# Optimization experiments

Measured on AMD Instinct MI355X. Metric: run time of the kernel, lower is better.

The kernel has to match this reference:

```python
import jax, jax.numpy as jnp
import numpy as np
from jax import lax

B_, CIN, COUT, H, W = 8, 64, 64, 64, 64
DIN, DSTATE, K, DTRANK = 128, 16, 4, 4  # d_inner=2*C, d_state=16, 4 scan dirs, dt_rank=ceil(64/16)


def setup_inputs():
    key = jax.random.key(0)
    ks = jax.random.split(key, 10)
    f = lambda k, s, sc=0.02: jax.random.normal(k, s, jnp.float32) * sc
    return {
        "x": jax.random.normal(ks[0], (B_, CIN, H, W), jnp.float32),
        "conv_w": f(ks[1], (COUT, CIN, 3, 3)),
        "conv_b": jnp.zeros((COUT,), jnp.float32),
        "gn_g": jnp.ones((COUT,), jnp.float32),
        "gn_b": jnp.zeros((COUT,), jnp.float32),
        "ln1_g": jnp.ones((COUT,), jnp.float32),
        "ln1_b": jnp.zeros((COUT,), jnp.float32),
        "in_proj_w": f(ks[2], (COUT, 2 * DIN)),
        "dw_w": f(ks[3], (DIN, 1, 3, 3)),
        "dw_b": jnp.zeros((DIN,), jnp.float32),
        "x_proj_w": f(ks[4], (K, DTRANK + 2 * DSTATE, DIN)),
        "dt_w": f(ks[5], (K, DIN, DTRANK)),
        "dt_b": f(ks[6], (K, DIN), 0.01),
        "A_logs": jnp.tile(jnp.log(jnp.arange(1, DSTATE + 1, dtype=jnp.float32)), (K, DIN, 1)),
        "Ds": jnp.ones((K, DIN), jnp.float32),
        "out_norm_g": jnp.ones((DIN,), jnp.float32),
        "out_norm_b": jnp.zeros((DIN,), jnp.float32),
        "out_proj_w": f(ks[7], (DIN, COUT)),
    }


def _ln(x, g, b, eps=1e-5):
    m = x.mean(-1, keepdims=True)
    v = ((x - m) ** 2).mean(-1, keepdims=True)
    return (x - m) * lax.rsqrt(v + eps) * g + b


def reference(x, conv_w, conv_b, gn_g, gn_b, ln1_g, ln1_b, in_proj_w, dw_w, dw_b,
              x_proj_w, dt_w, dt_b, A_logs, Ds, out_norm_g, out_norm_b, out_proj_w):
    # BasicConv2d: conv3x3 (stride 1, pad 1) + GroupNorm(2) + SiLU
    y = lax.conv_general_dilated(x, conv_w, (1, 1), [(1, 1), (1, 1)],
                                 dimension_numbers=("NCHW", "OIHW", "NCHW"))
    y = y + conv_b[None, :, None, None]
    Bb, C, Hh, Ww = y.shape
    yg = y.reshape(Bb, 2, C // 2, Hh, Ww)
    m = yg.mean((2, 3, 4), keepdims=True)
    v = ((yg - m) ** 2).mean((2, 3, 4), keepdims=True)
    y = ((yg - m) * lax.rsqrt(v + 1e-5)).reshape(Bb, C, Hh, Ww)
    y = y * gn_g[None, :, None, None] + gn_b[None, :, None, None]
    y = jax.nn.silu(y)
    # VSSBlock on NHWC: LN -> SS2D -> residual
    xb = y.transpose(0, 2, 3, 1)                       # (B,H,W,C)
    h = _ln(xb, ln1_g, ln1_b)
    xz = h @ in_proj_w                                 # (B,H,W,2*DIN)
    xm, z = jnp.split(xz, 2, axis=-1)
    xm = xm.transpose(0, 3, 1, 2)                      # (B,DIN,H,W)
    xm = lax.conv_general_dilated(xm, dw_w, (1, 1), [(1, 1), (1, 1)],
                                  dimension_numbers=("NCHW", "OIHW", "NCHW"),
                                  feature_group_count=DIN)
    xm = jax.nn.silu(xm + dw_b[None, :, None, None])
    L = Hh * Ww
    x1 = xm.reshape(Bb, DIN, L)                        # HW order
    x2 = xm.transpose(0, 1, 3, 2).reshape(Bb, DIN, L)  # WH order
    xs = jnp.stack([x1, x2], 1)
    xs = jnp.concatenate([xs, jnp.flip(xs, -1)], 1)    # (B,4,DIN,L)
    xdbl = jnp.einsum("bkdl,kcd->bkcl", xs, x_proj_w)
    dts, Bs, Cs = jnp.split(xdbl, [DTRANK, DTRANK + DSTATE], axis=2)
    dts = jnp.einsum("bkrl,kdr->bkdl", dts, dt_w)
    dt = jax.nn.softplus(dts + dt_b[None, :, :, None])  # (B,4,DIN,L)
    A = -jnp.exp(A_logs)                                # (K,DIN,DSTATE)
    # selective scan over L (time-major)
    u_t = xs.transpose(3, 0, 1, 2)
    dt_t = dt.transpose(3, 0, 1, 2)
    B_t = Bs.transpose(3, 0, 1, 2)
    C_t = Cs.transpose(3, 0, 1, 2)

    def step(hst, inp):
        u, d, Bc, Cc = inp
        hst = hst * jnp.exp(d[..., None] * A) + (d * u)[..., None] * Bc[:, :, None, :]
        return hst, jnp.einsum("bkdn,bkn->bkd", hst, Cc)

    h0 = jnp.zeros((Bb, K, DIN, DSTATE), xs.dtype)
    _, ys = lax.scan(step, h0, (u_t, dt_t, B_t, C_t))  # ys: (L,B,4,DIN)
    out_y = ys.transpose(1, 2, 3, 0) + Ds[None, :, :, None] * xs
    inv_y = jnp.flip(out_y[:, 2:4], -1)
    wh_y = out_y[:, 1].reshape(Bb, DIN, Ww, Hh).transpose(0, 1, 3, 2).reshape(Bb, DIN, L)
    invwh_y = inv_y[:, 1].reshape(Bb, DIN, Ww, Hh).transpose(0, 1, 3, 2).reshape(Bb, DIN, L)
    yv = out_y[:, 0] + inv_y[:, 0] + wh_y + invwh_y    # (B,DIN,L)
    yv = yv.transpose(0, 2, 1).reshape(Bb, Hh, Ww, DIN)
    yv = _ln(yv, out_norm_g, out_norm_b)
    yv = yv * jax.nn.silu(z)
    vss = xb + yv @ out_proj_w                          # VSSBlock residual
    return vss.transpose(0, 3, 1, 2) + y                # MambaDU residual
```

## Files before the change

### kernel.cpp

```cpp
#include <hip/hip_runtime.h>
#include <hip/hip_bf16.h>

#define BD   8
#define CD   64
#define HD   64
#define WD   64
#define LD   4096
#define DINN 128
#define KDIR 4
#define NST  16
#define L2E  1.442695040888963f

typedef const float* fp;

__device__ __forceinline__ float sigm(float x) { return 1.f / (1.f + __expf(-x)); }
__device__ __forceinline__ float softplusf(float x) {
    float e = __expf(-fabsf(x));
    return fmaxf(x, 0.f) + __logf(1.f + e);
}
__device__ __forceinline__ int pmap(int k, int l) {
    int m = (k & 2) ? (LD - 1 - l) : l;
    return (k & 1) ? (((m & 63) << 6) | (m >> 6)) : m;
}

__global__ __launch_bounds__(256) void k_conv(fp x, fp cw, fp cb, float* conv_out, float* gstats) {
    __shared__ float xt[64][3][68];
    __shared__ float red[4][4];
    int bx = blockIdx.x; int b = bx >> 6; int h = bx & 63;
    int t = threadIdx.x;
    for (int idx = t; idx < 64 * 3 * 64; idx += 256) {
        int ci = idx / 192, rem = idx % 192, r = rem >> 6, w = rem & 63;
        int hs = h + r - 1;
        float v = 0.f;
        if (hs >= 0 && hs < 64) v = x[((b * 64 + ci) * 64 + hs) * 64 + w];
        xt[ci][r][w + 1] = v;
    }
    for (int idx = t; idx < 64 * 3; idx += 256) {
        int ci = idx / 3, r = idx % 3;
        xt[ci][r][0] = 0.f; xt[ci][r][65] = 0.f; xt[ci][r][66] = 0.f; xt[ci][r][67] = 0.f;
    }
    __syncthreads();
    int co = t & 63, wq = t >> 6;
    float acc[16];
#pragma unroll
    for (int j = 0; j < 16; j++) acc[j] = 0.f;
    for (int ci = 0; ci < 64; ci++) {
        float wv[9];
        fp wp = cw + (co * 64 + ci) * 9;
#pragma unroll
        for (int q = 0; q < 9; q++) wv[q] = wp[q];
#pragma unroll
        for (int r = 0; r < 3; r++) {
            const float* row = &xt[ci][r][wq * 16];
            float xw[20];
#pragma unroll
            for (int q = 0; q < 5; q++) {
                float4 f = ((const float4*)row)[q];
                xw[4 * q] = f.x; xw[4 * q + 1] = f.y; xw[4 * q + 2] = f.z; xw[4 * q + 3] = f.w;
            }
#pragma unroll
            for (int j = 0; j < 16; j++)
                acc[j] += wv[r * 3 + 0] * xw[j] + wv[r * 3 + 1] * xw[j + 1] + wv[r * 3 + 2] * xw[j + 2];
        }
    }
    float bias = cb[co];
    __syncthreads();
    float* ot = &xt[0][0][0];
#pragma unroll
    for (int j = 0; j < 16; j++) ot[co * 64 + wq * 16 + j] = acc[j] + bias;
    __syncthreads();
    float ps0 = 0.f, pq0 = 0.f, ps1 = 0.f, pq1 = 0.f;
    for (int idx = t; idx < 4096; idx += 256) {
        int c2 = idx >> 6, w2 = idx & 63;
        float v = ot[idx];
        conv_out[((b * 64 + c2) * 64 + h) * 64 + w2] = v;
        bool g0 = c2 < 32;
        float v2 = v * v;
        ps0 += g0 ? v : 0.f; pq0 += g0 ? v2 : 0.f;
        ps1 += g0 ? 0.f : v; pq1 += g0 ? 0.f : v2;
    }
#pragma unroll
    for (int off = 32; off; off >>= 1) {
        ps0 += __shfl_xor(ps0, off); pq0 += __shfl_xor(pq0, off);
        ps1 += __shfl_xor(ps1, off); pq1 += __shfl_xor(pq1, off);
    }
    int wid = t >> 6;
    if ((t & 63) == 0) { red[wid][0] = ps0; red[wid][1] = pq0; red[wid][2] = ps1; red[wid][3] = pq1; }
    __syncthreads();
    if (t < 4) {
        float v = red[0][t] + red[1][t] + red[2][t] + red[3][t];
        atomicAdd(&gstats[b * 4 + t], v);
    }
}

__global__ __launch_bounds__(256) void k_gnapply(const float* conv_out, const float* gstats,
                                                 fp gng, fp gnb, float* y_nhwc) {
    __shared__ float tile[64][65];
    int bx = blockIdx.x; int b = bx >> 6; int p0 = (bx & 63) * 64;
    int t = threadIdx.x;
    const float invN = 1.f / (32.f * 4096.f);
    float s0 = gstats[b * 4 + 0], q0 = gstats[b * 4 + 1];
    float s1 = gstats[b * 4 + 2], q1 = gstats[b * 4 + 3];
    float m0 = s0 * invN, r0 = rsqrtf(q0 * invN - m0 * m0 + 1e-5f);
    float m1 = s1 * invN, r1 = rsqrtf(q1 * invN - m1 * m1 + 1e-5f);
    for (int idx = t; idx < 4096; idx += 256) {
        int c = idx >> 6, pi = idx & 63;
        float v = conv_out[(b * 64 + c) * LD + p0 + pi];
        float mean = (c < 32) ? m0 : m1, rstd = (c < 32) ? r0 : r1;
        v = (v - mean) * rstd * gng[c] + gnb[c];
        v = v * sigm(v);
        tile[c][pi] = v;
    }
    __syncthreads();
    for (int idx = t; idx < 4096; idx += 256) {
        int pi = idx >> 6, c = idx & 63;
        y_nhwc[(b * LD + p0 + pi) * 64 + c] = tile[c][pi];
    }
}

__global__ __launch_bounds__(256) void k_lninproj(const float* y_nhwc, fp lng, fp lnb, fp ipw,
                                                  float* xmc, float* zsil) {
    __shared__ float hn[4][64];
    int bp0 = blockIdx.x * 4;
    int t = threadIdx.x;
    int pix = t >> 6, lane = t & 63;
    {
        float v = y_nhwc[(bp0 + pix) * 64 + lane];
        float s = v, s2 = v * v;
#pragma unroll
        for (int off = 32; off; off >>= 1) { s += __shfl_xor(s, off); s2 += __shfl_xor(s2, off); }
        float mean = s * (1.f / 64.f);
        float rstd = rsqrtf(s2 * (1.f / 64.f) - mean * mean + 1e-5f);
        hn[pix][lane] = (v - mean) * rstd * lng[lane] + lnb[lane];
    }
    __syncthreads();
    float a0 = 0.f, a1 = 0.f, a2 = 0.f, a3 = 0.f;
    for (int c = 0; c < 64; c++) {
        float w = ipw[c * 256 + t];
        a0 += hn[0][c] * w; a1 += hn[1][c] * w; a2 += hn[2][c] * w; a3 += hn[3][c] * w;
    }
    float accv[4] = {a0, a1, a2, a3};
#pragma unroll
    for (int p = 0; p < 4; p++) {
        int bp = bp0 + p;
        float v = accv[p];
        if (t < 128) xmc[bp * 128 + t] = v;
        else         zsil[bp * 128 + (t - 128)] = v * sigm(v);
    }
}

__global__ __launch_bounds__(256) void k_dwconv(const float* xmc, fp dww, fp dwb, float* xm_dw) {
    int id = blockIdx.x * 256 + threadIdx.x;
    int d = id & 127, p = (id >> 7) & (LD - 1), b = id >> 19;
    int h = p >> 6, w = p & 63;
    float wv[9];
#pragma unroll
    for (int q = 0; q < 9; q++) wv[q] = dww[d * 9 + q];
    float acc = dwb[d];
#pragma unroll
    for (int i = 0; i < 3; i++) {
        int hs = h + i - 1; if (hs < 0 || hs > 63) continue;
#pragma unroll
        for (int j = 0; j < 3; j++) {
            int ws = w + j - 1; if (ws < 0 || ws > 63) continue;
            acc += xmc[((b << 12) + (hs << 6) + ws) * 128 + d] * wv[i * 3 + j];
        }
    }
    acc = acc * sigm(acc);
    xm_dw[id] = acc;
}

__global__ __launch_bounds__(192) void k_proj(const float* xm_dw, fp xpw, float* dts4, float* xBC) {
    __shared__ float u_lds[64 * 130];
    __shared__ float w_lds[128 * 40];
    int bx = blockIdx.x;
    int lt = bx & 63; int bk = bx >> 6; int k = bk & 3; int b = bk >> 2;
    int l0 = lt * 64;
    int t = threadIdx.x;
    for (int idx = t; idx < 36 * 128; idx += 192) {
        int c = idx % 36, d = idx / 36;
        w_lds[d * 40 + c] = xpw[(k * 36 + c) * 128 + d];
    }
    for (int idx = t; idx < 64 * 128; idx += 192) {
        int l = idx >> 7, d = idx & 127;
        u_lds[l * 130 + d] = xm_dw[(b * LD + pmap(k, l0 + l)) * 128 + d];
    }
    __syncthreads();
    int l = t & 63, cg = t >> 6;
    float acc[12];
#pragma unroll
    for (int i = 0; i < 12; i++) acc[i] = 0.f;
    for (int d = 0; d < 128; d++) {
        float uv = u_lds[l * 130 + d];
        const float* wr = &w_lds[d * 40 + cg * 12];
#pragma unroll
        for (int q = 0; q < 3; q++) {
            float4 f = ((const float4*)wr)[q];
            acc[4 * q + 0] += f.x * uv;
            acc[4 * q + 1] += f.y * uv;
            acc[4 * q + 2] += f.z * uv;
            acc[4 * q + 3] += f.w * uv;
        }
    }
    int base = bk * LD + l0 + l;
#pragma unroll
    for (int i = 0; i < 12; i++) {
        int c = cg * 12 + i;
        if (c < 4) dts4[base * 4 + c] = acc[i];
        else       xBC[base * 32 + (c - 4)] = acc[i];
    }
}

__global__ __launch_bounds__(128) void k_scan1(const float* xm_dw, const float* dts4, const float* xBC,
                                               fp dtw, fp dtbp, fp alog,
                                               float* Pbuf, float* Hbuf, int NCr, int CLr) {
    __shared__ float s_b[64 * 16];
    __shared__ float s_d4[64 * 4];
    int c = blockIdx.x, k = blockIdx.y, b = blockIdx.z;
    int d = threadIdx.x;
    int bk = b * 4 + k;
    int kd = k * 128 + d;
    float w0 = dtw[kd * 4 + 0], w1 = dtw[kd * 4 + 1], w2 = dtw[kd * 4 + 2], w3 = dtw[kd * 4 + 3];
    float dtb = dtbp[kd];
    float base = -__expf(alog[kd * 16]) * L2E;
    float A2[16];
    bool geo = true;
#pragma unroll
    for (int n = 0; n < 16; n++) {
        A2[n] = -__expf(alog[kd * 16 + n]) * L2E;
        float ideal = (float)(n + 1) * base;
        geo = geo && (fabsf(A2[n] - ideal) <= 1e-4f * fabsf(ideal));
    }
    float h[16]; float sdt = 0.f;
#pragma unroll
    for (int n = 0; n < 16; n++) h[n] = 0.f;
    int l0 = c * CLr;
    for (int ss = 0; ss < CLr; ss += 64) {
        if (ss) __syncthreads();
        int ls = l0 + ss;
        const float4* gd = (const float4*)&dts4[(size_t)(bk * LD + ls) * 4];
        if (d < 64) ((float4*)s_d4)[d] = gd[d];
        const float4* gx = (const float4*)&xBC[(size_t)(bk * LD + ls) * 32];
        for (int i = d; i < 64 * 4; i += 128) { int s = i >> 2, q = i & 3; ((float4*)s_b)[i] = gx[s * 8 + q]; }
        __syncthreads();
        int pbase = pmap(k, ls);
        int pstep = pmap(k, ls + 1) - pbase;
        const float* up = xm_dw + (size_t)(b * LD + pbase) * 128 + d;
        long ustep = (long)pstep * 128;
        if (geo) {
#pragma unroll 4
            for (int s = 0; s < 64; s++) {
                float4 dv = ((const float4*)s_d4)[s];
                float dtv = softplusf(dv.x * w0 + dv.y * w1 + dv.z * w2 + dv.w * w3 + dtb);
                sdt += dtv;
                float u = *up; up += ustep;
                float du = dtv * u;
                const float4* Bp = (const float4*)&s_b[s * 16];
                float4 B0 = Bp[0], B1 = Bp[1], B2 = Bp[2], B3 = Bp[3];
                float r = exp2f(dtv * base);
                float r2 = r * r, r3 = r2 * r, r4 = r2 * r2;
                float r5 = r4 * r, r6 = r4 * r2, r7 = r4 * r3, r8 = r4 * r4;
                float r9 = r8 * r, r10 = r8 * r2, r11 = r8 * r3, r12 = r8 * r4;
                float r13 = r8 * r5, r14 = r8 * r6, r15 = r8 * r7, r16 = r8 * r8;
                h[0]  = r   * h[0]  + du * B0.x;  h[1]  = r2  * h[1]  + du * B0.y;
                h[2]  = r3  * h[2]  + du * B0.z;  h[3]  = r4  * h[3]  + du * B0.w;
                h[4]  = r5  * h[4]  + du * B1.x;  h[5]  = r6  * h[5]  + du * B1.y;
                h[6]  = r7  * h[6]  + du * B1.z;  h[7]  = r8  * h[7]  + du * B1.w;
                h[8]  = r9  * h[8]  + du * B2.x;  h[9]  = r10 * h[9]  + du * B2.y;
                h[10] = r11 * h[10] + du * B2.z;  h[11] = r12 * h[11] + du * B2.w;
                h[12] = r13 * h[12] + du * B3.x;  h[13] = r14 * h[13] + du * B3.y;
                h[14] = r15 * h[14] + du * B3.z;  h[15] = r16 * h[15] + du * B3.w;
            }
        } else {
#pragma unroll 2
            for (int s = 0; s < 64; s++) {
                float4 dv = ((const float4*)s_d4)[s];
                float dtv = softplusf(dv.x * w0 + dv.y * w1 + dv.z * w2 + dv.w * w3 + dtb);
                sdt += dtv;
                float u = *up; up += ustep;
                float du = dtv * u;
                const float* Bp = &s_b[s * 16];
#pragma unroll
                for (int n = 0; n < 16; n++) {
                    float a = exp2f(dtv * A2[n]);
                    h[n] = a * h[n] + du * Bp[n];
                }
            }
        }
    }
    int obase = (bk * NCr + c) * 2048 + d;
#pragma unroll
    for (int n = 0; n < 16; n++) {
        Pbuf[obase + n * 128] = exp2f(sdt * A2[n]);
        Hbuf[obase + n * 128] = h[n];
    }
}

__global__ __launch_bounds__(256) void k_scan2(const float* Pbuf, const float* Hbuf, float* Hinit, int NCr) {
    int id = blockIdx.x * 256 + threadIdx.x;
    int nd = id & 2047; int bk = id >> 11;
    float h = 0.f;
    int base = bk * NCr * 2048 + nd;
    for (int c = 0; c < NCr; c++) {
        int idx = base + c * 2048;
        Hinit[idx] = h;
        h = Hbuf[idx] + Pbuf[idx] * h;
    }
}

__global__ __launch_bounds__(128) void k_scan3(const float* xm_dw, const float* dts4, const float* xBC,
                                               fp dtw, fp dtbp, fp alog, fp dsp,
                                               const float* Hinit, float* yv, int NCr, int CLr) {
    __shared__ float s_bc[64 * 32];
    __shared__ float s_d4[64 * 4];
    int c = blockIdx.x, k = blockIdx.y, b = blockIdx.z;
    int d = threadIdx.x;
    int bk = b * 4 + k;
    int kd = k * 128 + d;
    float w0 = dtw[kd * 4 + 0], w1 = dtw[kd * 4 + 1], w2 = dtw[kd * 4 + 2], w3 = dtw[kd * 4 + 3];
    float dtb = dtbp[kd];
    float Dv = dsp[kd];
    float base = -__expf(alog[kd * 16]) * L2E;
    float A2[16];
    bool geo = true;
#pragma unroll
    for (int n = 0; n < 16; n++) {
        A2[n] = -__expf(alog[kd * 16 + n]) * L2E;
        float ideal = (float)(n + 1) * base;
        geo = geo && (fabsf(A2[n] - ideal) <= 1e-4f * fabsf(ideal));
    }
    int hbase = (bk * NCr + c) * 2048 + d;
    float h[16];
#pragma unroll
    for (int n = 0; n < 16; n++) h[n] = Hinit[hbase + n * 128];
    int l0 = c * CLr;
    for (int ss = 0; ss < CLr; ss += 64) {
        if (ss) __syncthreads();
        int ls = l0 + ss;
        const float4* gd = (const float4*)&dts4[(size_t)(bk * LD + ls) * 4];
        if (d < 64) ((float4*)s_d4)[d] = gd[d];
        const float4* gx = (const float4*)&xBC[(size_t)(bk * LD + ls) * 32];
        for (int i = d; i < 64 * 8; i += 128) ((float4*)s_bc)[i] = gx[i];
        __syncthreads();
        int pbase = pmap(k, ls);
        int pstep = pmap(k, ls + 1) - pbase;
        const float* up = xm_dw + (size_t)(b * LD + pbase) * 128 + d;
        float* yp = yv + (size_t)(b * LD + pbase) * 128 + d;
        long ustep = (long)pstep * 128;
        if (geo) {
#pragma unroll 4
            for (int s = 0; s < 64; s++) {
                float4 dv = ((const float4*)s_d4)[s];
                float dtv = softplusf(dv.x * w0 + dv.y * w1 + dv.z * w2 + dv.w * w3 + dtb);
                float u = *up; up += ustep;
                float du = dtv * u;
                const float4* Bp = (const float4*)&s_bc[s * 32];
                float4 B0 = Bp[0], B1 = Bp[1], B2 = Bp[2], B3 = Bp[3];
                float4 C0 = Bp[4], C1 = Bp[5], C2 = Bp[6], C3 = Bp[7];
                float r = exp2f(dtv * base);
                float r2 = r * r, r3 = r2 * r, r4 = r2 * r2;
                float r5 = r4 * r, r6 = r4 * r2, r7 = r4 * r3, r8 = r4 * r4;
                float r9 = r8 * r, r10 = r8 * r2, r11 = r8 * r3, r12 = r8 * r4;
                float r13 = r8 * r5, r14 = r8 * r6, r15 = r8 * r7, r16 = r8 * r8;
                float y;
                h[0]  = r   * h[0]  + du * B0.x;  y  = h[0]  * C0.x;
                h[1]  = r2  * h[1]  + du * B0.y;  y += h[1]  * C0.y;
                h[2]  = r3  * h[2]  + du * B0.z;  y += h[2]  * C0.z;
                h[3]  = r4  * h[3]  + du * B0.w;  y += h[3]  * C0.w;
                h[4]  = r5  * h[4]  + du * B1.x;  y += h[4]  * C1.x;
                h[5]  = r6  * h[5]  + du * B1.y;  y += h[5]  * C1.y;
                h[6]  = r7  * h[6]  + du * B1.z;  y += h[6]  * C1.z;
                h[7]  = r8  * h[7]  + du * B1.w;  y += h[7]  * C1.w;
                h[8]  = r9  * h[8]  + du * B2.x;  y += h[8]  * C2.x;
                h[9]  = r10 * h[9]  + du * B2.y;  y += h[9]  * C2.y;
                h[10] = r11 * h[10] + du * B2.z;  y += h[10] * C2.z;
                h[11] = r12 * h[11] + du * B2.w;  y += h[11] * C2.w;
                h[12] = r13 * h[12] + du * B3.x;  y += h[12] * C3.x;
                h[13] = r14 * h[13] + du * B3.y;  y += h[13] * C3.y;
                h[14] = r15 * h[14] + du * B3.z;  y += h[14] * C3.z;
                h[15] = r16 * h[15] + du * B3.w;  y += h[15] * C3.w;
                y += Dv * u;
                atomicAdd(yp, y); yp += ustep;
            }
        } else {
#pragma unroll 2
            for (int s = 0; s < 64; s++) {
                float4 dv = ((const float4*)s_d4)[s];
                float dtv = softplusf(dv.x * w0 + dv.y * w1 + dv.z * w2 + dv.w * w3 + dtb);
                float u = *up; up += ustep;
                float du = dtv * u;
                const float* Bp = &s_bc[s * 32];
                float y = 0.f;
#pragma unroll
                for (int n = 0; n < 16; n++) {
                    float a = exp2f(dtv * A2[n]);
                    h[n] = a * h[n] + du * Bp[n];
                    y += h[n] * Bp[16 + n];
                }
                y += Dv * u;
                atomicAdd(yp, y); yp += ustep;
            }
        }
    }
}

__global__ __launch_bounds__(256) void k_final(const float* yv, const float* zsil, const float* y_nhwc,
                                               fp ong, fp onb, fp opw, float* out) {
    __shared__ float ylds[2][128];
    __shared__ float red[2][2][2];
    __shared__ float part[2][2][64];
    int bp0 = blockIdx.x * 2;
    int t = threadIdx.x;
    int pix = t >> 7, tl = t & 127;
    int bp = bp0 + pix;
    float v = yv[bp * 128 + tl];
    float s = v, s2 = v * v;
#pragma unroll
    for (int off = 32; off; off >>= 1) { s += __shfl_xor(s, off); s2 += __shfl_xor(s2, off); }
    int wh = (t >> 6) & 1;
    if ((t & 63) == 0) { red[pix][wh][0] = s; red[pix][wh][1] = s2; }
    __syncthreads();
    float S = red[pix][0][0] + red[pix][1][0], S2 = red[pix][0][1] + red[pix][1][1];
    float mean = S * (1.f / 128.f);
    float rstd = rsqrtf(S2 * (1.f / 128.f) - mean * mean + 1e-5f);
    float vn = (v - mean) * rstd * ong[tl] + onb[tl];
    vn *= zsil[bp * 128 + tl];
    ylds[pix][tl] = vn;
    __syncthreads();
    {
        int px = t >> 7, half = (t >> 6) & 1, co = t & 63;
        float acc = 0.f;
        const float* yrow = &ylds[px][half * 64];
        const float* wcol = &opw[half * 64 * 64 + co];
#pragma unroll 16
        for (int dd = 0; dd < 64; dd++) acc += yrow[dd] * wcol[dd * 64];
        part[px][half][co] = acc;
    }
    __syncthreads();
    if (t < 128) {
        int pp = t >> 6, co = t & 63;
        int bpo = bp0 + pp;
        float a = part[pp][0][co] + part[pp][1][co];
        float yb = y_nhwc[bpo * 64 + co];
        out[((bpo >> 12) * 64 + co) * LD + (bpo & 4095)] = 2.f * yb + a;
    }
}

extern "C" void kernel_launch(void* const* d_in, const int* in_sizes, int n_in,
                              void* d_out, int out_size, void* d_ws, size_t ws_size,
                              hipStream_t stream) {
    fp x    = (fp)d_in[0];
    fp cw   = (fp)d_in[1];
    fp cb   = (fp)d_in[2];
    fp gng  = (fp)d_in[3];
    fp gnb  = (fp)d_in[4];
    fp lng  = (fp)d_in[5];
    fp lnb  = (fp)d_in[6];
    fp ipw  = (fp)d_in[7];
    fp dww  = (fp)d_in[8];
    fp dwb  = (fp)d_in[9];
    fp xpw  = (fp)d_in[10];
    fp dtw  = (fp)d_in[11];
    fp dtb  = (fp)d_in[12];
    fp alog = (fp)d_in[13];
    fp dsp  = (fp)d_in[14];
    fp ong  = (fp)d_in[15];
    fp onb  = (fp)d_in[16];
    fp opw  = (fp)d_in[17];

    float* w = (float*)d_ws;
    float* conv_out = w;  w += BD * 64 * LD;
    float* y_nhwc   = w;  w += BD * LD * 64;
    float* gstats   = w;  w += 32;
    float* xmc      = w;  w += BD * LD * 128;
    float* zsil     = w;  w += BD * LD * 128;
    float* xm_dw    = w;  w += BD * LD * 128;
    float* dts4     = w;  w += BD * KDIR * LD * 4;
    float* xBC      = w;  w += BD * KDIR * LD * 32;
    float* yv       = w;  w += BD * LD * 128;
    size_t base_floats = (size_t)(w - (float*)d_ws);

    int NCr = 32;
    size_t perbuf64 = (size_t)32 * 64 * 2048;
    float *Pbuf, *Hbuf, *Hinit;
    if (ws_size >= (base_floats + 3 * perbuf64) * sizeof(float)) {
        NCr = 64;
        Pbuf  = w;  w += perbuf64;
        Hbuf  = w;  w += perbuf64;
        Hinit = w;  w += perbuf64;
    } else {
        Pbuf  = xmc;
        Hbuf  = xmc + (size_t)32 * 32 * 2048;
        Hinit = conv_out;
    }
    int CLr = LD / NCr;
    if (ws_size < base_floats * sizeof(float)) return;

    hipMemsetAsync(gstats, 0, 32 * sizeof(float), stream);
    k_conv<<<BD * HD, 256, 0, stream>>>(x, cw, cb, conv_out, gstats);
    k_gnapply<<<BD * 64, 256, 0, stream>>>(conv_out, gstats, gng, gnb, y_nhwc);
    k_lninproj<<<BD * LD / 4, 256, 0, stream>>>(y_nhwc, lng, lnb, ipw, xmc, zsil);
    k_dwconv<<<BD * LD * 128 / 256, 256, 0, stream>>>(xmc, dww, dwb, xm_dw);
    k_proj<<<BD * KDIR * 64, 192, 0, stream>>>(xm_dw, xpw, dts4, xBC);
    k_scan1<<<dim3(NCr, KDIR, BD), 128, 0, stream>>>(xm_dw, dts4, xBC, dtw, dtb, alog, Pbuf, Hbuf, NCr, CLr);
    k_scan2<<<256, 256, 0, stream>>>(Pbuf, Hbuf, Hinit, NCr);
    hipMemsetAsync(yv, 0, (size_t)BD * LD * 128 * sizeof(float), stream);
    k_scan3<<<dim3(NCr, KDIR, BD), 128, 0, stream>>>(xm_dw, dts4, xBC, dtw, dtb, alog, dsp, Hinit, yv, NCr, CLr);
    k_final<<<BD * LD / 2, 256, 0, stream>>>(yv, zsil, y_nhwc, ong, onb, opw, (float*)d_out);
}
```

Baseline: 447.4 us.

## Retile 3x3 conv to 4x4 channel-by-pixel register blocks with transposed weights

Adds a small kernel that transposes the conv weights into [ci][tap][co] order so each thread can load four output channels' weights with one float4. The conv thread mapping changes from one output channel by 16 pixels to four output channels by 4 pixels, which reuses each loaded input value across four channels. Outputs are written straight to global memory as float4 without staging through shared memory, so one sync pass is dropped. The cost is an extra kernel launch and a workspace buffer, and each thread now reads nine float4 weight values per input channel.

Result: no change. 452.6 us (+1.2%).

```diff
diff --git a/kernel.cpp b/kernel.cpp
--- a/kernel.cpp
+++ b/kernel.cpp
@@ -23,7 +23,14 @@
     return (k & 1) ? (((m & 63) << 6) | (m >> 6)) : m;
 }
 
-__global__ __launch_bounds__(256) void k_conv(fp x, fp cw, fp cb, float* conv_out, float* gstats) {
+__global__ __launch_bounds__(256) void k_wt(fp cw, float* wt) {
+    int id = blockIdx.x * 256 + threadIdx.x;
+    if (id >= 64 * 64 * 9) return;
+    int co = id & 63; int ciq = id >> 6; int ci = ciq / 9; int q = ciq % 9;
+    wt[id] = cw[(co * 64 + ci) * 9 + q];
+}
+
+__global__ __launch_bounds__(256) void k_conv(fp x, const float* wt, fp cb, float* conv_out, float* gstats) {
     __shared__ float xt[64][3][68];
     __shared__ float red[4][4];
     int bx = blockIdx.x; int b = bx >> 6; int h = bx & 63;
@@ -40,44 +47,44 @@
         xt[ci][r][0] = 0.f; xt[ci][r][65] = 0.f; xt[ci][r][66] = 0.f; xt[ci][r][67] = 0.f;
     }
     __syncthreads();
-    int co = t & 63, wq = t >> 6;
-    float acc[16];
-#pragma unroll
-    for (int j = 0; j < 16; j++) acc[j] = 0.f;
+    int coq = t & 15, wq = t >> 4;
+    float acc[4][4];
+#pragma unroll
+    for (int c = 0; c < 4; c++)
+#pragma unroll
+        for (int j = 0; j < 4; j++) acc[c][j] = 0.f;
     for (int ci = 0; ci < 64; ci++) {
-        float wv[9];
-        fp wp = cw + (co * 64 + ci) * 9;
-#pragma unroll
-        for (int q = 0; q < 9; q++) wv[q] = wp[q];
+        float4 wv[9];
+#pragma unroll
+        for (int q = 0; q < 9; q++) wv[q] = *(const float4*)&wt[(ci * 9 + q) * 64 + coq * 4];
 #pragma unroll
         for (int r = 0; r < 3; r++) {
-            const float* row = &xt[ci][r][wq * 16];
-            float xw[20];
-#pragma unroll
-            for (int q = 0; q < 5; q++) {
-                float4 f = ((const float4*)row)[q];
-                xw[4 * q] = f.x; xw[4 * q + 1] = f.y; xw[4 * q + 2] = f.z; xw[4 * q + 3] = f.w;
+            const float* row = &xt[ci][r][wq * 4];
+            float4 f0 = ((const float4*)row)[0], f1 = ((const float4*)row)[1];
+            float xr[8] = {f0.x, f0.y, f0.z, f0.w, f1.x, f1.y, f1.z, f1.w};
+            float4 wa = wv[r * 3 + 0], wb = wv[r * 3 + 1], wc = wv[r * 3 + 2];
+#pragma unroll
+            for (int j = 0; j < 4; j++) {
+                acc[0][j] += wa.x * xr[j] + wb.x * xr[j + 1] + wc.x * xr[j + 2];
+                acc[1][j] += wa.y * xr[j] + wb.y * xr[j + 1] + wc.y * xr[j + 2];
+                acc[2][j] += wa.z * xr[j] + wb.z * xr[j + 1] + wc.z * xr[j + 2];
+                acc[3][j] += wa.w * xr[j] + wb.w * xr[j + 1] + wc.w * xr[j + 2];
             }
-#pragma unroll
-            for (int j = 0; j < 16; j++)
-                acc[j] += wv[r * 3 + 0] * xw[j] + wv[r * 3 + 1] * xw[j + 1] + wv[r * 3 + 2] * xw[j + 2];
         }
     }
-    float bias = cb[co];
-    __syncthreads();
-    float* ot = &xt[0][0][0];
-#pragma unroll
-    for (int j = 0; j < 16; j++) ot[co * 64 + wq * 16 + j] = acc[j] + bias;
-    __syncthreads();
     float ps0 = 0.f, pq0 = 0.f, ps1 = 0.f, pq1 = 0.f;
-    for (int idx = t; idx < 4096; idx += 256) {
-        int c2 = idx >> 6, w2 = idx & 63;
-        float v = ot[idx];
-        conv_out[((b * 64 + c2) * 64 + h) * 64 + w2] = v;
-        bool g0 = c2 < 32;
-        float v2 = v * v;
-        ps0 += g0 ? v : 0.f; pq0 += g0 ? v2 : 0.f;
-        ps1 += g0 ? 0.f : v; pq1 += g0 ? 0.f : v2;
+    bool g0 = coq < 8;
+#pragma unroll
+    for (int cc = 0; cc < 4; cc++) {
+        int co = coq * 4 + cc;
+        float bias = cb[co];
+        float4 o;
+        o.x = acc[cc][0] + bias; o.y = acc[cc][1] + bias;
+        o.z = acc[cc][2] + bias; o.w = acc[cc][3] + bias;
+        *(float4*)&conv_out[((b * 64 + co) * 64 + h) * 64 + wq * 4] = o;
+        float s = o.x + o.y + o.z + o.w;
+        float q2 = o.x * o.x + o.y * o.y + o.z * o.z + o.w * o.w;
+        if (g0) { ps0 += s; pq0 += q2; } else { ps1 += s; pq1 += q2; }
     }
 #pragma unroll
     for (int off = 32; off; off >>= 1) {
@@ -472,6 +479,7 @@
     float* conv_out = w;  w += BD * 64 * LD;
     float* y_nhwc   = w;  w += BD * LD * 64;
     float* gstats   = w;  w += 32;
+    float* wt       = w;  w += 64 * 64 * 9;
     float* xmc      = w;  w += BD * LD * 128;
     float* zsil     = w;  w += BD * LD * 128;
     float* xm_dw    = w;  w += BD * LD * 128;
@@ -497,7 +505,8 @@
     if (ws_size < base_floats * sizeof(float)) return;
 
     hipMemsetAsync(gstats, 0, 32 * sizeof(float), stream);
-    k_conv<<<BD * HD, 256, 0, stream>>>(x, cw, cb, conv_out, gstats);
+    k_wt<<<144, 256, 0, stream>>>(cw, wt);
+    k_conv<<<BD * HD, 256, 0, stream>>>(x, wt, cb, conv_out, gstats);
     k_gnapply<<<BD * 64, 256, 0, stream>>>(conv_out, gstats, gng, gnb, y_nhwc);
     k_lninproj<<<BD * LD / 4, 256, 0, stream>>>(y_nhwc, lng, lnb, ipw, xmc, zsil);
     k_dwconv<<<BD * LD * 128 / 256, 256, 0, stream>>>(xmc, dww, dwb, xm_dw);
```
